# Kernel tuning notes

Measured on AMD Instinct MI355X. Metric: run time of the kernel, lower is better.

The kernel has to match this reference:

```python
import jax, jax.numpy as jnp
import numpy as np
from jax import lax

B, T, U, V = 4, 200, 100, 1024
D_ENC, D_DEC, J = 144, 320, 320


def setup_inputs() -> dict:
    key = jax.random.key(0)
    ks = jax.random.split(key, 8)
    s = lambda d: 1.0 / np.sqrt(d).astype(np.float32)
    return {
        "enc_out": jax.random.normal(ks[0], (B, T, D_ENC), jnp.float32),
        "dec_out": jax.random.normal(ks[1], (B, U + 1, D_DEC), jnp.float32),
        "W_enc": jax.random.normal(ks[2], (D_ENC, J), jnp.float32) * s(D_ENC),
        "b_enc": jnp.zeros((J,), jnp.float32),
        "W_dec": jax.random.normal(ks[3], (D_DEC, J), jnp.float32) * s(D_DEC),
        "b_dec": jnp.zeros((J,), jnp.float32),
        "W_out": jax.random.normal(ks[4], (J, V), jnp.float32) * s(J),
        "b_out": jnp.zeros((V,), jnp.float32),
        "targets": jax.random.randint(ks[5], (B, U), 1, V, jnp.int32),
        "enc_lengths": jax.random.randint(ks[6], (B,), T // 2, T + 1, jnp.int32),
        "target_lengths": jax.random.randint(ks[7], (B,), U // 2, U + 1, jnp.int32),
    }


def _rnnt_loss(log_probs, targets, enc_lengths, target_lengths):
    # log_probs: [B, T, U+1, V]; blank index = 0 (matches RNNTLoss(blank=0))
    blank_lp = log_probs[..., 0]  # [B, T, U+1]
    idx = jnp.broadcast_to(targets[:, None, :, None].astype(jnp.int32), (B, T, U, 1))
    emit_lp = jnp.take_along_axis(log_probs[:, :, :U, :], idx, axis=-1)[..., 0]  # [B, T, U]

    # alpha[0, u] = sum of emit log-probs along u at t=0
    alpha0 = jnp.concatenate(
        [jnp.zeros((B, 1), log_probs.dtype), jnp.cumsum(emit_lp[:, 0, :], axis=1)], axis=1
    )  # [B, U+1]

    def row(a, emit_t):
        # a: alpha_prev + blank (vertical transitions), [B, U+1]; emit_t: [B, U]
        def step(prev, xs):
            a_u, e_prev = xs
            cur = jnp.logaddexp(a_u, prev + e_prev)
            return cur, cur
        _, rest = lax.scan(step, a[:, 0], (a[:, 1:].T, emit_t.T))  # rest: [U, B]
        return jnp.concatenate([a[:, :1], rest.T], axis=1)

    def t_step(alpha_prev, xs):
        blank_prev, emit_t = xs
        alpha_t = row(alpha_prev + blank_prev, emit_t)
        return alpha_t, alpha_t

    xs = (jnp.swapaxes(blank_lp[:, :-1, :], 0, 1), jnp.swapaxes(emit_lp[:, 1:, :], 0, 1))
    _, alphas_rest = lax.scan(t_step, alpha0, xs)  # [T-1, B, U+1]
    alphas = jnp.concatenate([alpha0[None], alphas_rest], axis=0)  # [T, B, U+1]

    b_idx = jnp.arange(B)
    t_idx = enc_lengths - 1
    ll = alphas[t_idx, b_idx, target_lengths] + blank_lp[b_idx, t_idx, target_lengths]
    return jnp.mean(-ll)  # reduction='mean' over batch


def reference(enc_out, dec_out, W_enc, b_enc, W_dec, b_dec, W_out, b_out, targets, enc_lengths, target_lengths):
    enc_p = enc_out @ W_enc + b_enc  # [B, T, J]
    dec_p = dec_out @ W_dec + b_dec  # [B, U+1, J]
    joint = jnp.tanh(enc_p[:, :, None, :] + dec_p[:, None, :, :])  # [B, T, U+1, J]
    logits = joint @ W_out + b_out  # [B, T, U+1, V]
    log_probs = jax.nn.log_softmax(logits, axis=-1)
    return _rnnt_loss(log_probs, targets, enc_lengths, target_lengths)
```

## Files before the change

### kernel.cpp

```cpp
#include <hip/hip_runtime.h>
#include <hip/hip_bf16.h>
#include <math.h>

#define B_ 4
#define T_ 200
#define U_ 100
#define V_ 1024
#define DE 144
#define DD 320
#define J_ 320
#define M_TOT (B_ * T_ * (U_ + 1))
#define SSTR 328
#define DSTR 104
#define NDIAG 300
#define LOG2E 1.4426950408889634f
#define LN2 0.6931471805599453f

typedef __attribute__((ext_vector_type(8))) short bf16x8_t;
typedef __attribute__((ext_vector_type(4))) float f32x4_t;

__device__ __forceinline__ float fast_tanh(float x) {
    float e = exp2f(x * (2.0f * LOG2E));
    float r = __frcp_rn(e + 1.0f);
    return fmaf(-2.0f, r, 1.0f);
}

__device__ __forceinline__ ushort f2bf(float x) {
    uint u = __float_as_uint(x);
    uint r = (u + 0x7FFFu + ((u >> 16) & 1u)) >> 16;
    return (ushort)r;
}

template <int K>
__device__ __forceinline__ void proj_body(const float* __restrict__ X,
                                          const float* __restrict__ W,
                                          const float* __restrict__ bias,
                                          float* __restrict__ Y,
                                          int r0, int R, float* sx, int tid) {
    constexpr int QK = K / 4;
    for (int q = tid; q < 16 * QK; q += 640) {
        int row = q / QK;
        int kq = q - row * QK;
        int r = r0 + row;
        if (r >= R) r = R - 1;
        *(float4*)&sx[row * K + kq * 4] = *(const float4*)&X[r * K + kq * 4];
    }
    __syncthreads();
    const int half = (tid >= 320) ? 1 : 0;
    const int c = tid - half * 320;
    float acc[8];
#pragma unroll
    for (int i = 0; i < 8; i++) acc[i] = 0.0f;
    for (int k = 0; k < K; k += 4) {
        float w0 = W[(k + 0) * 320 + c];
        float w1 = W[(k + 1) * 320 + c];
        float w2 = W[(k + 2) * 320 + c];
        float w3 = W[(k + 3) * 320 + c];
#pragma unroll
        for (int i = 0; i < 8; i++) {
            const float4 x4 = *(const float4*)&sx[(half * 8 + i) * K + k];
            acc[i] = fmaf(x4.x, w0, acc[i]);
            acc[i] = fmaf(x4.y, w1, acc[i]);
            acc[i] = fmaf(x4.z, w2, acc[i]);
            acc[i] = fmaf(x4.w, w3, acc[i]);
        }
    }
    const float bb = bias[c];
#pragma unroll
    for (int i = 0; i < 8; i++) {
        int r = r0 + half * 8 + i;
        if (r < R) Y[r * 320 + c] = acc[i] + bb;
    }
}

__global__ __launch_bounds__(640) void prep_kernel(
    const float* __restrict__ enc_out, const float* __restrict__ dec_out,
    const float* __restrict__ W_enc, const float* __restrict__ b_enc,
    const float* __restrict__ W_dec, const float* __restrict__ b_dec,
    const float* __restrict__ W_out,
    float* __restrict__ enc_p, float* __restrict__ dec_p,
    ushort* __restrict__ Wt) {
    __shared__ float sx[16 * 320];
    const int bid = blockIdx.x;
    const int tid = threadIdx.x;
    if (bid < 50) {
        proj_body<DE>(enc_out, W_enc, b_enc, enc_p, bid * 16, B_ * T_, sx, tid);
    } else if (bid < 76) {
        proj_body<DD>(dec_out, W_dec, b_dec, dec_p, (bid - 50) * 16,
                      B_ * (U_ + 1), sx, tid);
    } else {
        int idx = (bid - 76) * 640 + tid;
        int k = idx >> 10;
        int v = idx & 1023;
        ushort b = f2bf(W_out[idx]);
        int frag = (v >> 4) * 10 + (k >> 5);
        int lane = (v & 15) | (((k >> 3) & 3) << 4);
        int elem = k & 7;
        Wt[frag * 512 + lane * 8 + elem] = b;
    }
}

__global__ __launch_bounds__(1024, 4) void joint_mfma(
    const float* __restrict__ enc_p, const float* __restrict__ dec_p,
    const ushort* __restrict__ Wt, const float* __restrict__ b_out,
    const int* __restrict__ targets,
    float* __restrict__ bsk, float* __restrict__ esk) {
    __shared__ ushort sh[64 * SSTR];
    __shared__ float parts[16][64];
    __shared__ float lse_sh[64];
    __shared__ int tgt_sh[64];

    const int tid = threadIdx.x;
    const int r0 = blockIdx.x * 64;

    if (tid < 64) {
        int rc = r0 + tid;
        int tg = -1;
        if (rc < M_TOT) {
            int b = rc / 20200;
            int rem = rc - b * 20200;
            int u = rem - (rem / 101) * 101;
            if (u < U_) tg = targets[b * U_ + u];
        }
        tgt_sh[tid] = tg;
    }

    {
        const int si = tid >> 4;
        const int sq = tid & 15;
        int rc = r0 + si;
        if (rc > M_TOT - 1) rc = M_TOT - 1;
        int b = rc / 20200;
        int rem = rc - b * 20200;
        int t = rem / 101;
        int u = rem - t * 101;
        const float4* ep = (const float4*)&enc_p[(b * 200 + t) * 320];
        const float4* dp = (const float4*)&dec_p[(b * 101 + u) * 320];
        ushort* shp = &sh[si * SSTR];
#pragma unroll
        for (int it = 0; it < 5; it++) {
            int kq = sq + it * 16;
            float4 e = ep[kq];
            float4 dd = dp[kq];
            float t0 = fast_tanh(e.x + dd.x);
            float t1 = fast_tanh(e.y + dd.y);
            float t2 = fast_tanh(e.z + dd.z);
            float t3 = fast_tanh(e.w + dd.w);
            __hip_bfloat162 p0 = __float22bfloat162_rn(make_float2(t0, t1));
            __hip_bfloat162 p1 = __float22bfloat162_rn(make_float2(t2, t3));
            uint2 pk;
            pk.x = *(uint*)&p0;
            pk.y = *(uint*)&p1;
            *(uint2*)&shp[kq * 4] = pk;
        }
    }
    __syncthreads();

    const int wave = tid >> 6;
    const int lane = tid & 63;
    const int lrow = lane & 15;
    const int lk = (lane >> 4) * 8;
    const int cb16 = wave * 4;

    f32x4_t acc[4][4];
#pragma unroll
    for (int mt = 0; mt < 4; mt++)
#pragma unroll
        for (int nt = 0; nt < 4; nt++) acc[mt][nt] = (f32x4_t)(0.0f);

    bf16x8_t bnx[4];
#pragma unroll
    for (int nt = 0; nt < 4; nt++)
        bnx[nt] = *(const bf16x8_t*)&Wt[(((cb16 + nt) * 10 + 0) << 9) + lane * 8];
    for (int ks = 0; ks < 10; ks++) {
        bf16x8_t a[4];
#pragma unroll
        for (int mt = 0; mt < 4; mt++)
            a[mt] = *(const bf16x8_t*)&sh[(mt * 16 + lrow) * SSTR + ks * 32 + lk];
        bf16x8_t bc[4];
#pragma unroll
        for (int nt = 0; nt < 4; nt++) bc[nt] = bnx[nt];
        if (ks < 9) {
#pragma unroll
            for (int nt = 0; nt < 4; nt++)
                bnx[nt] = *(const bf16x8_t*)&Wt[(((cb16 + nt) * 10 + ks + 1) << 9) + lane * 8];
        }
#pragma unroll
        for (int nt = 0; nt < 4; nt++) {
            __builtin_amdgcn_s_setprio(1);
#pragma unroll
            for (int mt = 0; mt < 4; mt++)
                acc[mt][nt] = __builtin_amdgcn_mfma_f32_16x16x32_bf16(a[mt], bc[nt], acc[mt][nt], 0, 0, 0);
            __builtin_amdgcn_s_setprio(0);
        }
    }

    float bo[4];
#pragma unroll
    for (int nt = 0; nt < 4; nt++) bo[nt] = b_out[wave * 64 + nt * 16 + lrow];
#pragma unroll
    for (int mt = 0; mt < 4; mt++)
#pragma unroll
        for (int nt = 0; nt < 4; nt++) acc[mt][nt] += bo[nt];

#pragma unroll
    for (int mt = 0; mt < 4; mt++) {
#pragma unroll
        for (int j = 0; j < 4; j++) {
            float s = exp2f(acc[mt][0][j] * LOG2E);
            s += exp2f(acc[mt][1][j] * LOG2E);
            s += exp2f(acc[mt][2][j] * LOG2E);
            s += exp2f(acc[mt][3][j] * LOG2E);
#pragma unroll
            for (int off = 1; off < 16; off <<= 1)
                s += __shfl_xor(s, off, 16);
            if (lrow == 0) {
                int row = mt * 16 + (lane >> 4) * 4 + j;
                parts[wave][row] = s;
            }
        }
    }
    __syncthreads();
    if (tid < 64) {
        float s = parts[0][tid];
#pragma unroll
        for (int w = 1; w < 16; w++) s += parts[w][tid];
        lse_sh[tid] = __log2f(s) * LN2;
    }
    __syncthreads();

#pragma unroll
    for (int mt = 0; mt < 4; mt++) {
#pragma unroll
        for (int j = 0; j < 4; j++) {
            int lr = mt * 16 + (lane >> 4) * 4 + j;
            int r = r0 + lr;
            if (r >= M_TOT) continue;
            int tc = tgt_sh[lr];
            bool isblank = (wave == 0) && (lrow == 0);
            bool isemit = (tc >= 0) && ((tc >> 6) == wave) && ((tc & 15) == lrow);
            if (isblank || isemit) {
                int b = r / 20200;
                int rem = r - b * 20200;
                int t = rem / 101;
                int u = rem - t * 101;
                float lse = lse_sh[lr];
                if (isblank)
                    bsk[(b * NDIAG + t + u) * DSTR + u] = acc[mt][0][j] - lse;
                if (isemit) {
                    int ntl = (tc >> 4) & 3;
                    float v = acc[mt][0][j];
#pragma unroll
                    for (int nt = 1; nt < 4; nt++)
                        if (nt == ntl) v = acc[mt][nt][j];
                    esk[(b * NDIAG + t + u) * DSTR + u] = v - lse;
                }
            }
        }
    }
}

__global__ __launch_bounds__(256, 1) void alpha_c2_kernel(
    const float* __restrict__ bsk, const float* __restrict__ esk,
    const int* __restrict__ enc_len, const int* __restrict__ tgt_len,
    float* __restrict__ out) {
    __shared__ float ll_sh[B_];
    const int tid = threadIdx.x;
    const int b = tid >> 6;
    const int l = tid & 63;
    const float* Bp = bsk + b * (NDIAG * DSTR);
    const float* Ep = esk + b * (NDIAG * DSTR);
    const int el = enc_len[b];
    const int tl = tgt_len[b];
    const int dfin = el - 1 + tl;

    const int u0 = 2 * l;
    const bool ok0 = (u0 <= U_);
    const bool ok1 = (u0 + 1 <= U_);
    const int uc = ok0 ? u0 : 0;

    float A0 = (l == 0) ? 0.0f : -INFINITY;
    float A1 = -INFINITY;

    float2 rb[8], re[8];
#pragma unroll
    for (int k = 0; k < 8; k++) {
        rb[k] = *(const float2*)&Bp[k * DSTR + uc];
        re[k] = *(const float2*)&Ep[k * DSTR + uc];
    }

    for (int dc = 1; dc <= 297; dc += 8) {
#pragma unroll
        for (int q = 0; q < 8; q++) {
            const int d = dc + q;
            if (d > NDIAG - 1) continue;
            const int sc = q;
            const int sm = (q + 1) & 7;
            float2 cb = rb[sc], ce = re[sc];
            float2 mb = rb[sm];
            int dn = d + 7;
            if (dn > NDIAG - 1) dn = NDIAG - 1;
            rb[sc] = *(const float2*)&Bp[dn * DSTR + uc];
            re[sc] = *(const float2*)&Ep[dn * DSTR + uc];

            float s = A1 + ce.y;
            float sn = __shfl_up(s, 1, 64);

            float va0 = A0 + cb.x;
            float vb0 = (l >= 1) ? sn : -INFINITY;
            float va1 = A1 + cb.y;
            float vb1 = A0 + ce.x;

            float M0 = fmaxf(va0, vb0);
            float n0 = (M0 == -INFINITY)
                           ? -INFINITY
                           : M0 + __logf(1.0f + __expf(fminf(va0, vb0) - M0));
            float M1 = fmaxf(va1, vb1);
            float n1 = (M1 == -INFINITY)
                           ? -INFINITY
                           : M1 + __logf(1.0f + __expf(fminf(va1, vb1) - M1));

            const int t0 = d - u0;
            if (!ok0 || t0 < 0 || t0 >= T_) n0 = -INFINITY;
            if (!ok1 || (t0 - 1) < 0 || (t0 - 1) >= T_) n1 = -INFINITY;

            if (d == dfin) {
                if (tl == u0) ll_sh[b] = n0 + mb.x;
                if (tl == u0 + 1) ll_sh[b] = n1 + mb.y;
            }
            A0 = n0;
            A1 = n1;
        }
    }
    __syncthreads();
    if (tid == 0)
        out[0] = -0.25f * (ll_sh[0] + ll_sh[1] + ll_sh[2] + ll_sh[3]);
}

extern "C" void kernel_launch(void* const* d_in, const int* in_sizes, int n_in,
                              void* d_out, int out_size, void* d_ws, size_t ws_size,
                              hipStream_t stream) {
    const float* enc_out = (const float*)d_in[0];
    const float* dec_out = (const float*)d_in[1];
    const float* W_enc = (const float*)d_in[2];
    const float* b_enc = (const float*)d_in[3];
    const float* W_dec = (const float*)d_in[4];
    const float* b_dec = (const float*)d_in[5];
    const float* W_out = (const float*)d_in[6];
    const float* b_out = (const float*)d_in[7];
    const int* targets = (const int*)d_in[8];
    const int* enc_len = (const int*)d_in[9];
    const int* tgt_len = (const int*)d_in[10];

    float* ws = (float*)d_ws;
    float* enc_p = ws;
    float* dec_p = enc_p + B_ * T_ * J_;
    float* bsk = dec_p + B_ * (U_ + 1) * J_;
    float* esk = bsk + B_ * NDIAG * DSTR;
    ushort* Wt = (ushort*)(esk + B_ * NDIAG * DSTR);

    prep_kernel<<<588, 640, 0, stream>>>(enc_out, dec_out, W_enc, b_enc,
                                         W_dec, b_dec, W_out, enc_p, dec_p, Wt);

    joint_mfma<<<(M_TOT + 63) / 64, 1024, 0, stream>>>(
        enc_p, dec_p, Wt, b_out, targets, bsk, esk);

    alpha_c2_kernel<<<1, 256, 0, stream>>>(bsk, esk, enc_len, tgt_len,
                                           (float*)d_out);
}
```

Baseline: 215.1 us.

## Fuse alpha recursion into joint kernel via last-block counter; use 512-thread blocks

Removes the separate single-block alpha kernel launch by having the last-finishing joint block, detected through an atomic counter that the prep kernel resets, run the RNNT alpha recursion. Separately, the joint GEMM block shrinks from 16 to 8 waves, each wave now covering 128 vocab columns with 32 accumulators. The B-fragment software prefetch is dropped and B is loaded inline. This saves one launch but adds threadfence and atomic overhead, and the heavier per-wave register load may lower occupancy.

After: 433.4 us. 2.02x slower.

```diff
diff --git a/kernel.cpp b/kernel.cpp
--- a/kernel.cpp
+++ b/kernel.cpp
@@ -10,6 +10,7 @@
 #define DD 320
 #define J_ 320
 #define M_TOT (B_ * T_ * (U_ + 1))
+#define NBLK 1263
 #define SSTR 328
 #define DSTR 104
 #define NDIAG 300
@@ -79,10 +80,11 @@
     const float* __restrict__ W_dec, const float* __restrict__ b_dec,
     const float* __restrict__ W_out,
     float* __restrict__ enc_p, float* __restrict__ dec_p,
-    ushort* __restrict__ Wt) {
+    ushort* __restrict__ Wt, int* __restrict__ counter) {
     __shared__ float sx[16 * 320];
     const int bid = blockIdx.x;
     const int tid = threadIdx.x;
+    if (bid == 0 && tid == 0) *counter = 0;
     if (bid < 50) {
         proj_body<DE>(enc_out, W_enc, b_enc, enc_p, bid * 16, B_ * T_, sx, tid);
     } else if (bid < 76) {
@@ -100,15 +102,19 @@
     }
 }
 
-__global__ __launch_bounds__(1024, 4) void joint_mfma(
+__global__ __launch_bounds__(512, 2) void joint_mfma(
     const float* __restrict__ enc_p, const float* __restrict__ dec_p,
     const ushort* __restrict__ Wt, const float* __restrict__ b_out,
     const int* __restrict__ targets,
-    float* __restrict__ bsk, float* __restrict__ esk) {
+    float* __restrict__ bsk, float* __restrict__ esk,
+    const int* __restrict__ enc_len, const int* __restrict__ tgt_len,
+    int* __restrict__ counter, float* __restrict__ out) {
     __shared__ ushort sh[64 * SSTR];
-    __shared__ float parts[16][64];
+    __shared__ float parts[8][64];
     __shared__ float lse_sh[64];
     __shared__ int tgt_sh[64];
+    __shared__ int flag_sh;
+    __shared__ float ll_sh[B_];
 
     const int tid = threadIdx.x;
     const int r0 = blockIdx.x * 64;
@@ -126,8 +132,8 @@
     }
 
     {
-        const int si = tid >> 4;
-        const int sq = tid & 15;
+        const int si = tid >> 3;
+        const int sq = tid & 7;
         int rc = r0 + si;
         if (rc > M_TOT - 1) rc = M_TOT - 1;
         int b = rc / 20200;
@@ -138,8 +144,8 @@
         const float4* dp = (const float4*)&dec_p[(b * 101 + u) * 320];
         ushort* shp = &sh[si * SSTR];
 #pragma unroll
-        for (int it = 0; it < 5; it++) {
-            int kq = sq + it * 16;
+        for (int it = 0; it < 10; it++) {
+            int kq = it * 8 + sq;
             float4 e = ep[kq];
             float4 dd = dp[kq];
             float t0 = fast_tanh(e.x + dd.x);
@@ -160,57 +166,45 @@
     const int lane = tid & 63;
     const int lrow = lane & 15;
     const int lk = (lane >> 4) * 8;
-    const int cb16 = wave * 4;
-
-    f32x4_t acc[4][4];
+    const int cb16 = wave * 8;
+
+    f32x4_t acc[4][8];
 #pragma unroll
     for (int mt = 0; mt < 4; mt++)
 #pragma unroll
-        for (int nt = 0; nt < 4; nt++) acc[mt][nt] = (f32x4_t)(0.0f);
-
-    bf16x8_t bnx[4];
-#pragma unroll
-    for (int nt = 0; nt < 4; nt++)
-        bnx[nt] = *(const bf16x8_t*)&Wt[(((cb16 + nt) * 10 + 0) << 9) + lane * 8];
+        for (int nt = 0; nt < 8; nt++) acc[mt][nt] = (f32x4_t)(0.0f);
+
     for (int ks = 0; ks < 10; ks++) {
         bf16x8_t a[4];
 #pragma unroll
         for (int mt = 0; mt < 4; mt++)
             a[mt] = *(const bf16x8_t*)&sh[(mt * 16 + lrow) * SSTR + ks * 32 + lk];
-        bf16x8_t bc[4];
-#pragma unroll
-        for (int nt = 0; nt < 4; nt++) bc[nt] = bnx[nt];
-        if (ks < 9) {
-#pragma unroll
-            for (int nt = 0; nt < 4; nt++)
-                bnx[nt] = *(const bf16x8_t*)&Wt[(((cb16 + nt) * 10 + ks + 1) << 9) + lane * 8];
-        }
-#pragma unroll
-        for (int nt = 0; nt < 4; nt++) {
+#pragma unroll
+        for (int nt = 0; nt < 8; nt++) {
+            bf16x8_t bfr = *(const bf16x8_t*)&Wt[(((cb16 + nt) * 10 + ks) << 9) + lane * 8];
             __builtin_amdgcn_s_setprio(1);
 #pragma unroll
             for (int mt = 0; mt < 4; mt++)
-                acc[mt][nt] = __builtin_amdgcn_mfma_f32_16x16x32_bf16(a[mt], bc[nt], acc[mt][nt], 0, 0, 0);
+                acc[mt][nt] = __builtin_amdgcn_mfma_f32_16x16x32_bf16(a[mt], bfr, acc[mt][nt], 0, 0, 0);
             __builtin_amdgcn_s_setprio(0);
         }
     }
 
-    float bo[4];
-#pragma unroll
-    for (int nt = 0; nt < 4; nt++) bo[nt] = b_out[wave * 64 + nt * 16 + lrow];
+    float bo[8];
+#pragma unroll
+    for (int nt = 0; nt < 8; nt++) bo[nt] = b_out[wave * 128 + nt * 16 + lrow];
 #pragma unroll
     for (int mt = 0; mt < 4; mt++)
 #pragma unroll
-        for (int nt = 0; nt < 4; nt++) acc[mt][nt] += bo[nt];
+        for (int nt = 0; nt < 8; nt++) acc[mt][nt] += bo[nt];
 
 #pragma unroll
     for (int mt = 0; mt < 4; mt++) {
 #pragma unroll
         for (int j = 0; j < 4; j++) {
-            float s = exp2f(acc[mt][0][j] * LOG2E);
-            s += exp2f(acc[mt][1][j] * LOG2E);
-            s += exp2f(acc[mt][2][j] * LOG2E);
-            s += exp2f(acc[mt][3][j] * LOG2E);
+            float s = 0.0f;
+#pragma unroll
+            for (int nt = 0; nt < 8; nt++) s += exp2f(acc[mt][nt][j] * LOG2E);
 #pragma unroll
             for (int off = 1; off < 16; off <<= 1)
                 s += __shfl_xor(s, off, 16);
@@ -224,7 +218,7 @@
     if (tid < 64) {
         float s = parts[0][tid];
 #pragma unroll
-        for (int w = 1; w < 16; w++) s += parts[w][tid];
+        for (int w = 1; w < 8; w++) s += parts[w][tid];
         lse_sh[tid] = __log2f(s) * LN2;
     }
     __syncthreads();
@@ -238,7 +232,7 @@
             if (r >= M_TOT) continue;
             int tc = tgt_sh[lr];
             bool isblank = (wave == 0) && (lrow == 0);
-            bool isemit = (tc >= 0) && ((tc >> 6) == wave) && ((tc & 15) == lrow);
+            bool isemit = (tc >= 0) && ((tc >> 7) == wave) && ((tc & 15) == lrow);
             if (isblank || isemit) {
                 int b = r / 20200;
                 int rem = r - b * 20200;
@@ -248,88 +242,90 @@
                 if (isblank)
                     bsk[(b * NDIAG + t + u) * DSTR + u] = acc[mt][0][j] - lse;
                 if (isemit) {
-                    int ntl = (tc >> 4) & 3;
+                    int ntl = (tc >> 4) & 7;
                     float v = acc[mt][0][j];
 #pragma unroll
-                    for (int nt = 1; nt < 4; nt++)
+                    for (int nt = 1; nt < 8; nt++)
                         if (nt == ntl) v = acc[mt][nt][j];
                     esk[(b * NDIAG + t + u) * DSTR + u] = v - lse;
                 }
             }
         }
     }
-}
-
-__global__ __launch_bounds__(256, 1) void alpha_c2_kernel(
-    const float* __restrict__ bsk, const float* __restrict__ esk,
-    const int* __restrict__ enc_len, const int* __restrict__ tgt_len,
-    float* __restrict__ out) {
-    __shared__ float ll_sh[B_];
-    const int tid = threadIdx.x;
-    const int b = tid >> 6;
-    const int l = tid & 63;
-    const float* Bp = bsk + b * (NDIAG * DSTR);
-    const float* Ep = esk + b * (NDIAG * DSTR);
-    const int el = enc_len[b];
-    const int tl = tgt_len[b];
-    const int dfin = el - 1 + tl;
-
-    const int u0 = 2 * l;
-    const bool ok0 = (u0 <= U_);
-    const bool ok1 = (u0 + 1 <= U_);
-    const int uc = ok0 ? u0 : 0;
-
-    float A0 = (l == 0) ? 0.0f : -INFINITY;
-    float A1 = -INFINITY;
-
-    float2 rb[8], re[8];
-#pragma unroll
-    for (int k = 0; k < 8; k++) {
-        rb[k] = *(const float2*)&Bp[k * DSTR + uc];
-        re[k] = *(const float2*)&Ep[k * DSTR + uc];
-    }
-
-    for (int dc = 1; dc <= 297; dc += 8) {
-#pragma unroll
-        for (int q = 0; q < 8; q++) {
-            const int d = dc + q;
-            if (d > NDIAG - 1) continue;
-            const int sc = q;
-            const int sm = (q + 1) & 7;
-            float2 cb = rb[sc], ce = re[sc];
-            float2 mb = rb[sm];
-            int dn = d + 7;
-            if (dn > NDIAG - 1) dn = NDIAG - 1;
-            rb[sc] = *(const float2*)&Bp[dn * DSTR + uc];
-            re[sc] = *(const float2*)&Ep[dn * DSTR + uc];
-
-            float s = A1 + ce.y;
-            float sn = __shfl_up(s, 1, 64);
-
-            float va0 = A0 + cb.x;
-            float vb0 = (l >= 1) ? sn : -INFINITY;
-            float va1 = A1 + cb.y;
-            float vb1 = A0 + ce.x;
-
-            float M0 = fmaxf(va0, vb0);
-            float n0 = (M0 == -INFINITY)
-                           ? -INFINITY
-                           : M0 + __logf(1.0f + __expf(fminf(va0, vb0) - M0));
-            float M1 = fmaxf(va1, vb1);
-            float n1 = (M1 == -INFINITY)
-                           ? -INFINITY
-                           : M1 + __logf(1.0f + __expf(fminf(va1, vb1) - M1));
-
-            const int t0 = d - u0;
-            if (!ok0 || t0 < 0 || t0 >= T_) n0 = -INFINITY;
-            if (!ok1 || (t0 - 1) < 0 || (t0 - 1) >= T_) n1 = -INFINITY;
-
-            if (d == dfin) {
-                if (tl == u0) ll_sh[b] = n0 + mb.x;
-                if (tl == u0 + 1) ll_sh[b] = n1 + mb.y;
+
+    __threadfence();
+    __syncthreads();
+    if (tid == 0) flag_sh = atomicAdd(counter, 1);
+    __syncthreads();
+    if (flag_sh != NBLK - 1) return;
+    __threadfence();
+
+    if (tid < 256) {
+        const int b = tid >> 6;
+        const int l = tid & 63;
+        const float* Bp = bsk + b * (NDIAG * DSTR);
+        const float* Ep = esk + b * (NDIAG * DSTR);
+        const int el = enc_len[b];
+        const int tl = tgt_len[b];
+        const int dfin = el - 1 + tl;
+
+        const int u0 = 2 * l;
+        const bool ok0 = (u0 <= U_);
+        const bool ok1 = (u0 + 1 <= U_);
+        const int uc = ok0 ? u0 : 0;
+
+        float A0 = (l == 0) ? 0.0f : -INFINITY;
+        float A1 = -INFINITY;
+
+        float2 rb[8], re[8];
+#pragma unroll
+        for (int k = 0; k < 8; k++) {
+            rb[k] = *(const float2*)&Bp[k * DSTR + uc];
+            re[k] = *(const float2*)&Ep[k * DSTR + uc];
+        }
+
+        for (int dc = 1; dc <= 297; dc += 8) {
+#pragma unroll
+            for (int q = 0; q < 8; q++) {
+                const int d = dc + q;
+                if (d > NDIAG - 1) continue;
+                const int sc = q;
+                const int sm = (q + 1) & 7;
+                float2 cb = rb[sc], ce = re[sc];
+                float2 mb = rb[sm];
+                int dn = d + 7;
+                if (dn > NDIAG - 1) dn = NDIAG - 1;
+                rb[sc] = *(const float2*)&Bp[dn * DSTR + uc];
+                re[sc] = *(const float2*)&Ep[dn * DSTR + uc];
+
+                float s = A1 + ce.y;
+                float sn = __shfl_up(s, 1, 64);
+
+                float va0 = A0 + cb.x;
+                float vb0 = (l >= 1) ? sn : -INFINITY;
+                float va1 = A1 + cb.y;
+                float vb1 = A0 + ce.x;
+
+                float M0 = fmaxf(va0, vb0);
+                float n0 = (M0 == -INFINITY)
+                               ? -INFINITY
+                               : M0 + __logf(1.0f + __expf(fminf(va0, vb0) - M0));
+                float M1 = fmaxf(va1, vb1);
+                float n1 = (M1 == -INFINITY)
+                               ? -INFINITY
+                               : M1 + __logf(1.0f + __expf(fminf(va1, vb1) - M1));
+
+                const int t0 = d - u0;
+                if (!ok0 || t0 < 0 || t0 >= T_) n0 = -INFINITY;
+                if (!ok1 || (t0 - 1) < 0 || (t0 - 1) >= T_) n1 = -INFINITY;
+
+                if (d == dfin) {
+                    if (tl == u0) ll_sh[b] = n0 + mb.x;
+                    if (tl == u0 + 1) ll_sh[b] = n1 + mb.y;
+                }
+                A0 = n0;
+                A1 = n1;
             }
-            A0 = n0;
-            A1 = n1;
         }
     }
     __syncthreads();
@@ -358,13 +354,13 @@
     float* bsk = dec_p + B_ * (U_ + 1) * J_;
     float* esk = bsk + B_ * NDIAG * DSTR;
     ushort* Wt = (ushort*)(esk + B_ * NDIAG * DSTR);
+    int* counter = (int*)(Wt + J_ * V_);
 
     prep_kernel<<<588, 640, 0, stream>>>(enc_out, dec_out, W_enc, b_enc,
-                                         W_dec, b_dec, W_out, enc_p, dec_p, Wt);
-
-    joint_mfma<<<(M_TOT + 63) / 64, 1024, 0, stream>>>(
-        enc_p, dec_p, Wt, b_out, targets, bsk, esk);
-
-    alpha_c2_kernel<<<1, 256, 0, stream>>>(bsk, esk, enc_len, tgt_len,
-                                           (float*)d_out);
-}
+                                         W_dec, b_dec, W_out, enc_p, dec_p, Wt,
+                                         counter);
+
+    joint_mfma<<<NBLK, 512, 0, stream>>>(enc_p, dec_p, Wt, b_out, targets,
+                                         bsk, esk, enc_len, tgt_len, counter,
+                                         (float*)d_out);
+}
```
